# Performance work log

Measured on AMD Instinct MI355X. Metric: run time of the kernel, lower is better.

Reference implementation:

```python
import jax, jax.numpy as jnp
import numpy as np

NEG_SLOPE = 0.2
N, E, NNZ, IN, H, C = 100000, 50000, 800000, 128, 8, 16


def setup_inputs() -> dict:
    key = jax.random.key(0)
    ks = jax.random.split(key, 8)
    X = jax.random.normal(ks[0], (N, IN), jnp.float32)
    W_typed = jax.random.normal(ks[1], (4, IN, H * C), jnp.float32) * (1.0 / np.sqrt(IN))
    att_e = jax.random.normal(ks[2], (4, H, C), jnp.float32) * 0.1
    att_v = jax.random.normal(ks[3], (4, H, C), jnp.float32) * 0.1
    vertex = jax.random.randint(ks[4], (NNZ,), 0, N, jnp.int32)
    edges = jax.random.randint(ks[5], (NNZ,), 0, E, jnp.int32)
    vtype = jax.random.randint(ks[6], (N,), 0, 4, jnp.int32)
    etype = jax.random.randint(ks[7], (E,), 0, 4, jnp.int32)
    return {"X": X, "W_typed": W_typed, "att_e": att_e, "att_v": att_v,
            "vertex": vertex, "edges": edges, "vtype": vtype, "etype": etype}


def _segment_softmax(logits, seg, num):
    # numerically-stable softmax over segments (PyG-style, eps in denominator)
    m = jax.ops.segment_max(logits, seg, num_segments=num)
    ex = jnp.exp(logits - m[seg])
    s = jax.ops.segment_sum(ex, seg, num_segments=num)
    return ex / (s[seg] + 1e-16)


def reference(X, W_typed, att_e, att_v, vertex, edges, vtype, etype):
    # typed linear: project with all 4 type weights, select per node type
    Xall = jnp.einsum('ni,tio->tno', X, W_typed)        # [4, N, H*C]
    X0 = Xall[vtype, jnp.arange(N)]                     # [N, H*C]
    Xn = X0.reshape(N, H, C)
    Xve = Xn[vertex]                                    # [NNZ, H, C] gather vertex->incidence
    # vertex->edge attention, typed by edge type of each incidence
    beta = jnp.sum(Xve * att_e[etype[edges]], axis=-1)  # [NNZ, H]
    beta = jax.nn.leaky_relu(beta, NEG_SLOPE)
    beta = _segment_softmax(beta, edges, E)
    Xe = jax.nn.relu(jax.ops.segment_sum(Xve * beta[..., None], edges, num_segments=E))  # [E, H, C]
    Xe = Xe[edges]                                      # [NNZ, H, C] gather edge->incidence
    # edge->vertex attention, typed by node type of each incidence's vertex
    alpha = jnp.sum(Xe * att_v[vtype[vertex]], axis=-1)  # [NNZ, H]
    alpha = jax.nn.leaky_relu(alpha, NEG_SLOPE)
    alpha = _segment_softmax(alpha, vertex, N)
    Xv = jax.ops.segment_sum(Xe * alpha[..., None], vertex, num_segments=N)  # [N, H, C]
    return Xv.reshape(N, H * C)
```

## Files before the change

kernel.cpp:

```cpp
#include <hip/hip_runtime.h>

typedef __attribute__((ext_vector_type(8))) short bf16x8;
typedef __attribute__((ext_vector_type(4))) float f32x4;

#define NEG_SLOPE 0.2f

__device__ __forceinline__ unsigned short f2bf(float f){
  unsigned u = __float_as_uint(f);
  u = (u + 0x7fffu + ((u >> 16) & 1u)) >> 16;
  return (unsigned short)u;
}
__device__ __forceinline__ float bflo(unsigned u){ return __uint_as_float(u << 16); }
__device__ __forceinline__ float bfhi(unsigned u){ return __uint_as_float(u & 0xffff0000u); }
__device__ __forceinline__ float lrelu(float x){ return x > 0.f ? x : NEG_SLOPE * x; }

__global__ __launch_bounds__(256) void k_histprep(
    const int* __restrict__ edges, const int* __restrict__ vertex, int NNZ,
    int* __restrict__ cnt, int E, int nbHist,
    const int* __restrict__ vtype, int N, int* __restrict__ tcnt, int nbHN,
    const float* __restrict__ W, short* __restrict__ Bfrag){
  __shared__ int lcnt[4];
  int b = (int)blockIdx.x;
  if (b < nbHist){
    int i = b * 256 + threadIdx.x;
    if (i < NNZ){
      atomicAdd(cnt + edges[i], 1);
      atomicAdd(cnt + E + vertex[i], 1);
    }
    return;
  }
  b -= nbHist;
  if (b < nbHN){
    if (threadIdx.x < 4) lcnt[threadIdx.x] = 0;
    __syncthreads();
    int i = b * 256 + threadIdx.x;
    if (i < N) atomicAdd(&lcnt[vtype[i]], 1);
    __syncthreads();
    if (threadIdx.x < 4 && lcnt[threadIdx.x] > 0)
      atomicAdd(tcnt + threadIdx.x, lcnt[threadIdx.x]);
    return;
  }
  b -= nbHN;
  int u = b * 256 + threadIdx.x;
  int j = u & 7, lane = (u >> 3) & 63, ct = (u >> 9) & 31, ks = u >> 14;
  int k = ks * 32 + ((lane >> 4) << 3) + j;
  int col = (ct << 4) + (lane & 15);
  int t = col >> 7, o = col & 127;
  Bfrag[u] = (short)f2bf(W[(t * 128 + k) * 128 + o]);
}

__global__ __launch_bounds__(256) void k_scanA(const int* __restrict__ cnt, int S,
                                               int* __restrict__ bsum){
  __shared__ int sh[256];
  int base = blockIdx.x * 1024 + threadIdx.x * 4;
  int s = 0;
  #pragma unroll
  for (int k = 0; k < 4; ++k){ int idx = base + k; if (idx < S) s += cnt[idx]; }
  sh[threadIdx.x] = s; __syncthreads();
  for (int off = 128; off > 0; off >>= 1){
    if (threadIdx.x < off) sh[threadIdx.x] += sh[threadIdx.x + off];
    __syncthreads();
  }
  if (threadIdx.x == 0) bsum[blockIdx.x] = sh[0];
}

__global__ void k_scanB(int* bsum, int nb, const int* __restrict__ tcnt,
                        int* __restrict__ pbase){
  if (threadIdx.x == 0 && blockIdx.x == 0){
    int run = 0;
    for (int b = 0; b < nb; ++b){ int v = bsum[b]; bsum[b] = run; run += v; }
    int pb = 0;
    for (int t = 0; t < 4; ++t){
      pbase[t] = pb;
      pb += ((tcnt[t] + 63) >> 6) << 6;
    }
    pbase[4] = pb;
  }
}

__global__ __launch_bounds__(256) void k_scanC(const int* __restrict__ cnt, int S,
    const int* __restrict__ bsum, int* __restrict__ offs, int* __restrict__ cursor,
    int nbS, const int* __restrict__ vtype, int N, const int* __restrict__ pbase,
    int* __restrict__ tcur, int* __restrict__ nsorted){
  __shared__ int sh[256];
  __shared__ int gbase[4];
  int t = threadIdx.x;
  int b = (int)blockIdx.x;
  if (b >= nbS){
    int* lcnt = sh;
    if (t < 4) lcnt[t] = 0;
    __syncthreads();
    int i = (b - nbS) * 256 + t;
    int tt = 0, rank = 0;
    bool valid = i < N;
    if (valid){ tt = vtype[i]; rank = atomicAdd(&lcnt[tt], 1); }
    __syncthreads();
    if (t < 4 && lcnt[t] > 0) gbase[t] = atomicAdd(tcur + t, lcnt[t]);
    __syncthreads();
    if (valid) nsorted[pbase[tt] + gbase[tt] + rank] = i;
    return;
  }
  int base = b * 1024 + t * 4;
  int c[4]; int s = 0;
  #pragma unroll
  for (int k = 0; k < 4; ++k){ int idx = base + k; c[k] = (idx < S) ? cnt[idx] : 0; s += c[k]; }
  sh[t] = s; __syncthreads();
  for (int off = 1; off < 256; off <<= 1){
    int v = (t >= off) ? sh[t - off] : 0; __syncthreads();
    sh[t] += v; __syncthreads();
  }
  int run = bsum[b] + sh[t] - s;
  #pragma unroll
  for (int k = 0; k < 4; ++k){
    int idx = base + k;
    if (idx < S){ offs[idx] = run; cursor[idx] = run; run += c[k]; }
  }
}

__global__ __launch_bounds__(256, 3) void k_gemm_place(const float* __restrict__ X,
    const short* __restrict__ Bfrag, const int* __restrict__ nsorted,
    const int* __restrict__ pbase, unsigned short* __restrict__ X0,
    const int* __restrict__ edges, const int* __restrict__ vertex, int NNZ,
    int* __restrict__ cursor, int* __restrict__ rows, int nbPlace){
  __shared__ short shB[8 * 4 * 64 * 8];
  const int tid = threadIdx.x;
  const int q = (int)blockIdx.x / 3, r = (int)blockIdx.x % 3;

  if (r != 0){
    int hb = 2 * q + (r - 1);
    if (hb < nbPlace){
      int i = hb * 256 + tid;
      if (i < NNZ){
        int pos = atomicAdd(cursor + edges[i], 1);
        rows[pos] = vertex[i];
      }
    }
    return;
  }

  const int rowIdx = q * 64;
  const int t = (rowIdx >= pbase[1]) + (rowIdx >= pbase[2]) + (rowIdx >= pbase[3]);

  const bf16x8* Bv = (const bf16x8*)Bfrag;
  bf16x8* shBv = (bf16x8*)shB;
  #pragma unroll
  for (int v = 0; v < 8; ++v){
    int item = v * 256 + tid;
    int slab = item >> 6, ln = item & 63;
    int ks = slab >> 3, ctl = slab & 7;
    shBv[item] = Bv[((ks * 32 + 8 * t + ctl) * 64) + ln];
  }

  const int w = tid >> 6, lane = tid & 63;
  const int m = lane & 15, qq = lane >> 4;
  const int node = nsorted[rowIdx + w * 16 + m];

  bf16x8 afrag[4];
  #pragma unroll
  for (int ks = 0; ks < 4; ++ks){
    bf16x8 f;
    if (node >= 0){
      const float4* src = (const float4*)(X + (size_t)node * 128 + ks * 32 + qq * 8);
      float4 a = src[0], b = src[1];
      f[0]=(short)f2bf(a.x); f[1]=(short)f2bf(a.y); f[2]=(short)f2bf(a.z); f[3]=(short)f2bf(a.w);
      f[4]=(short)f2bf(b.x); f[5]=(short)f2bf(b.y); f[6]=(short)f2bf(b.z); f[7]=(short)f2bf(b.w);
    } else {
      #pragma unroll
      for (int z = 0; z < 8; ++z) f[z] = 0;
    }
    afrag[ks] = f;
  }

  f32x4 acc[8];
  #pragma unroll
  for (int ct = 0; ct < 8; ++ct){
    acc[ct][0]=0.f; acc[ct][1]=0.f; acc[ct][2]=0.f; acc[ct][3]=0.f;
  }

  __syncthreads();
  #pragma unroll
  for (int ctl = 0; ctl < 8; ++ctl){
    #pragma unroll
    for (int ks = 0; ks < 4; ++ks){
      bf16x8 bf = shBv[(ks * 8 + ctl) * 64 + lane];
      acc[ctl] = __builtin_amdgcn_mfma_f32_16x16x32_bf16(afrag[ks], bf, acc[ctl], 0, 0, 0);
    }
  }

  const int col0 = lane & 15;
  #pragma unroll
  for (int rr = 0; rr < 4; ++rr){
    int row = nsorted[rowIdx + w * 16 + qq * 4 + rr];
    if (row < 0) continue;
    #pragma unroll
    for (int ctl = 0; ctl < 8; ++ctl)
      X0[(size_t)row * 128 + ctl * 16 + col0] = f2bf(acc[ctl][rr]);
  }
}

template<int OUT_BF16>
__device__ __forceinline__ void seg_body(const uint4* __restrict__ feat,
    const float* __restrict__ att, const int* __restrict__ rows_sorted,
    const int* __restrict__ offs, const int* __restrict__ cnt,
    const int* __restrict__ stype, void* __restrict__ outbuf,
    int S, int blockId, int tid){
  int wid = tid >> 6, lane = tid & 63;
  int s = blockId * 4 + wid;
  if (s >= S) return;
  int t = stype[s];
  int sub = lane >> 4, lane16 = lane & 15;
  const float4* ap = (const float4*)(att + t * 128 + lane16 * 8);
  float4 A0 = ap[0], A1 = ap[1];
  int start = offs[s], len = cnt[s];
  float denom = 0.f;
  float acc[8];
  #pragma unroll
  for (int e = 0; e < 8; ++e) acc[e] = 0.f;

  for (int base = 0; base < len; base += 64){
    int m = len - base; if (m > 64) m = 64;
    int idx = 0;
    if (lane < m) idx = rows_sorted[start + base + lane];
    int ng = (m + 3) >> 2;
    uint4 uA = make_uint4(0,0,0,0), uB = make_uint4(0,0,0,0);
    {
      int r0 = __shfl(idx, sub);
      if (sub < m) uA = feat[(size_t)r0 * 16 + lane16];
      int r1 = __shfl(idx, 4 + sub);
      if (4 + sub < m) uB = feat[(size_t)r1 * 16 + lane16];
    }
    for (int g = 0; g < ng; g += 2){
      {
        uint4 u = uA;
        int nr = (g + 2) * 4 + sub;
        int rn = __shfl(idx, nr & 63);
        if (nr < m) uA = feat[(size_t)rn * 16 + lane16];
        float x0 = bflo(u.x), x1 = bfhi(u.x), x2 = bflo(u.y), x3 = bfhi(u.y);
        float x4 = bflo(u.z), x5 = bfhi(u.z), x6 = bflo(u.w), x7 = bfhi(u.w);
        float p = x0*A0.x + x1*A0.y + x2*A0.z + x3*A0.w
                + x4*A1.x + x5*A1.y + x6*A1.z + x7*A1.w;
        p += __shfl_xor(p, 1);
        float wgt = __expf(lrelu(p));
        wgt = (g * 4 + sub < m) ? wgt : 0.f;
        denom += wgt;
        acc[0] += wgt*x0; acc[1] += wgt*x1; acc[2] += wgt*x2; acc[3] += wgt*x3;
        acc[4] += wgt*x4; acc[5] += wgt*x5; acc[6] += wgt*x6; acc[7] += wgt*x7;
      }
      if (g + 1 < ng){
        uint4 u = uB;
        int nr = (g + 3) * 4 + sub;
        int rn = __shfl(idx, nr & 63);
        if (nr < m) uB = feat[(size_t)rn * 16 + lane16];
        float x0 = bflo(u.x), x1 = bfhi(u.x), x2 = bflo(u.y), x3 = bfhi(u.y);
        float x4 = bflo(u.z), x5 = bfhi(u.z), x6 = bflo(u.w), x7 = bfhi(u.w);
        float p = x0*A0.x + x1*A0.y + x2*A0.z + x3*A0.w
                + x4*A1.x + x5*A1.y + x6*A1.z + x7*A1.w;
        p += __shfl_xor(p, 1);
        float wgt = __expf(lrelu(p));
        wgt = ((g + 1) * 4 + sub < m) ? wgt : 0.f;
        denom += wgt;
        acc[0] += wgt*x0; acc[1] += wgt*x1; acc[2] += wgt*x2; acc[3] += wgt*x3;
        acc[4] += wgt*x4; acc[5] += wgt*x5; acc[6] += wgt*x6; acc[7] += wgt*x7;
      }
    }
  }
  denom += __shfl_xor(denom, 16);
  denom += __shfl_xor(denom, 32);
  #pragma unroll
  for (int e = 0; e < 8; ++e){
    acc[e] += __shfl_xor(acc[e], 16);
    acc[e] += __shfl_xor(acc[e], 32);
  }
  float inv = 1.f / (denom + 1e-16f);
  float v[8];
  #pragma unroll
  for (int e = 0; e < 8; ++e) v[e] = acc[e] * inv;

  if constexpr (OUT_BF16){
    if (sub == 0){
      uint4 pw;
      pw.x = (unsigned)f2bf(fmaxf(v[0],0.f)) | ((unsigned)f2bf(fmaxf(v[1],0.f)) << 16);
      pw.y = (unsigned)f2bf(fmaxf(v[2],0.f)) | ((unsigned)f2bf(fmaxf(v[3],0.f)) << 16);
      pw.z = (unsigned)f2bf(fmaxf(v[4],0.f)) | ((unsigned)f2bf(fmaxf(v[5],0.f)) << 16);
      pw.w = (unsigned)f2bf(fmaxf(v[6],0.f)) | ((unsigned)f2bf(fmaxf(v[7],0.f)) << 16);
      ((uint4*)outbuf)[(size_t)s * 16 + lane16] = pw;
    }
  } else {
    if (sub == 0){
      float4* op = (float4*)outbuf;
      op[(size_t)s * 32 + lane16 * 2]     = make_float4(v[0], v[1], v[2], v[3]);
      op[(size_t)s * 32 + lane16 * 2 + 1] = make_float4(v[4], v[5], v[6], v[7]);
    }
  }
}

__global__ __launch_bounds__(256) void k_place_seg1(
    const int* __restrict__ edges, const int* __restrict__ vertex, int NNZ,
    int* __restrict__ cursor, int* __restrict__ rows, int E,
    int nbPlace, int nbSeg,
    const uint4* __restrict__ X0, const float* __restrict__ att_e,
    const int* __restrict__ offs, const int* __restrict__ cnt,
    const int* __restrict__ etype, void* __restrict__ Xe){
  const int q = (int)blockIdx.x / 5, r = (int)blockIdx.x % 5;
  if (r == 0){
    if (q < nbPlace){
      int i = q * 256 + threadIdx.x;
      if (i < NNZ){
        int pos = atomicAdd(cursor + E + vertex[i], 1);
        rows[pos] = edges[i];
      }
    }
    return;
  }
  int segBlk = q * 4 + (r - 1);
  if (segBlk >= nbSeg) return;
  seg_body<1>(X0, att_e, rows, offs, cnt, etype, Xe, E, segBlk, threadIdx.x);
}

__global__ __launch_bounds__(256) void k_seg2(const uint4* __restrict__ Xe,
    const float* __restrict__ att_v, const int* __restrict__ rows,
    const int* __restrict__ offs, const int* __restrict__ cnt,
    const int* __restrict__ vtype, float* __restrict__ out, int N){
  seg_body<0>(Xe, att_v, rows, offs, cnt, vtype, out, N,
              (int)blockIdx.x, threadIdx.x);
}

extern "C" void kernel_launch(void* const* d_in, const int* in_sizes, int n_in,
                              void* d_out, int out_size, void* d_ws, size_t ws_size,
                              hipStream_t stream){
  const float* X      = (const float*)d_in[0];
  const float* W      = (const float*)d_in[1];
  const float* att_e  = (const float*)d_in[2];
  const float* att_v  = (const float*)d_in[3];
  const int*   vertex = (const int*)d_in[4];
  const int*   edges  = (const int*)d_in[5];
  const int*   vtype  = (const int*)d_in[6];
  const int*   etype  = (const int*)d_in[7];
  float* out = (float*)d_out;
  const int N   = in_sizes[0] / 128;
  const int NNZ = in_sizes[4];
  const int E   = in_sizes[7];
  const int S   = E + N;

  const int nbI = (NNZ + 255) / 256;
  const int nbHN = (N + 255) / 256;
  const int nbS = (S + 1023) / 1024;
  const int nbSeg1 = (E + 3) / 4;
  const int nbPad = (N + 252 + 63) / 64;
  const int nsortedCap = nbPad * 64;

  char* wp = (char*)d_ws;
  int* cnt    = (int*)wp; wp += (size_t)S * 4;
  int* tcnt   = (int*)wp; wp += 16;
  int* tcur   = (int*)wp; wp += 16;
  int* offs   = (int*)wp; wp += (size_t)S * 4;
  int* cursor = (int*)wp; wp += (size_t)S * 4;
  int* bsum   = (int*)wp; wp += 1024;
  int* pbase  = (int*)wp; wp += 32;
  int* rows   = (int*)wp; wp += (size_t)2 * NNZ * 4;
  int* nsorted= (int*)wp; wp += (size_t)nsortedCap * 4;
  unsigned short* X0 = (unsigned short*)wp; wp += (size_t)N * 128 * 2;
  unsigned short* Xe = (unsigned short*)wp; wp += (size_t)E * 128 * 2;
  short* Bfrag = (short*)wp; wp += (size_t)65536 * 2;

  hipMemsetAsync(cnt, 0, (size_t)(S + 8) * 4, stream);
  hipMemsetAsync(nsorted, 0xFF, (size_t)nsortedCap * 4, stream);

  k_histprep<<<nbI + nbHN + 256, 256, 0, stream>>>(edges, vertex, NNZ, cnt, E,
      nbI, vtype, N, tcnt, nbHN, W, Bfrag);

  k_scanA<<<nbS, 256, 0, stream>>>(cnt, S, bsum);
  k_scanB<<<1, 64, 0, stream>>>(bsum, nbS, tcnt, pbase);
  k_scanC<<<nbS + nbHN, 256, 0, stream>>>(cnt, S, bsum, offs, cursor,
      nbS, vtype, N, pbase, tcur, nsorted);

  k_gemm_place<<<3 * nbPad, 256, 0, stream>>>(X, Bfrag, nsorted, pbase,
      (unsigned short*)X0, edges, vertex, NNZ, cursor, rows, nbI);

  k_place_seg1<<<5 * nbI, 256, 0, stream>>>(edges, vertex, NNZ, cursor,
      rows, E, nbI, nbSeg1, (const uint4*)X0, att_e, offs, cnt, etype, Xe);

  k_seg2<<<(N + 3) / 4, 256, 0, stream>>>((const uint4*)Xe, att_v,
      rows, offs + E, cnt + E, vtype, out, N);
}
```

Baseline: 346.5 us.

## Record histogram ranks during GEMM and place CSR rows without atomics

The edge/vertex histogram now runs alongside the typed-projection GEMM and records each incidence's atomic rank. A separate non-atomic placement kernel then writes rows from offset plus rank, replacing the cursor atomics that previously ran during GEMM and seg1. The node-type sort moves ahead of the GEMM, so the schedule gains kernels (prep, pbase, nodeplace, scan, place) and two NNZ-sized rank buffers. The aim is to drop one round of contended atomics and let the scan overlap less critical work, at the cost of extra launches and memory traffic.

```diff
diff --git a/kernel.cpp b/kernel.cpp
--- a/kernel.cpp
+++ b/kernel.cpp
@@ -14,22 +14,11 @@
 __device__ __forceinline__ float bfhi(unsigned u){ return __uint_as_float(u & 0xffff0000u); }
 __device__ __forceinline__ float lrelu(float x){ return x > 0.f ? x : NEG_SLOPE * x; }
 
-__global__ __launch_bounds__(256) void k_histprep(
-    const int* __restrict__ edges, const int* __restrict__ vertex, int NNZ,
-    int* __restrict__ cnt, int E, int nbHist,
+__global__ __launch_bounds__(256) void k_prep(
     const int* __restrict__ vtype, int N, int* __restrict__ tcnt, int nbHN,
     const float* __restrict__ W, short* __restrict__ Bfrag){
   __shared__ int lcnt[4];
   int b = (int)blockIdx.x;
-  if (b < nbHist){
-    int i = b * 256 + threadIdx.x;
-    if (i < NNZ){
-      atomicAdd(cnt + edges[i], 1);
-      atomicAdd(cnt + E + vertex[i], 1);
-    }
-    return;
-  }
-  b -= nbHist;
   if (b < nbHN){
     if (threadIdx.x < 4) lcnt[threadIdx.x] = 0;
     __syncthreads();
@@ -49,26 +38,8 @@
   Bfrag[u] = (short)f2bf(W[(t * 128 + k) * 128 + o]);
 }
 
-__global__ __launch_bounds__(256) void k_scanA(const int* __restrict__ cnt, int S,
-                                               int* __restrict__ bsum){
-  __shared__ int sh[256];
-  int base = blockIdx.x * 1024 + threadIdx.x * 4;
-  int s = 0;
-  #pragma unroll
-  for (int k = 0; k < 4; ++k){ int idx = base + k; if (idx < S) s += cnt[idx]; }
-  sh[threadIdx.x] = s; __syncthreads();
-  for (int off = 128; off > 0; off >>= 1){
-    if (threadIdx.x < off) sh[threadIdx.x] += sh[threadIdx.x + off];
-    __syncthreads();
-  }
-  if (threadIdx.x == 0) bsum[blockIdx.x] = sh[0];
-}
-
-__global__ void k_scanB(int* bsum, int nb, const int* __restrict__ tcnt,
-                        int* __restrict__ pbase){
+__global__ void k_pbase(const int* __restrict__ tcnt, int* __restrict__ pbase){
   if (threadIdx.x == 0 && blockIdx.x == 0){
-    int run = 0;
-    for (int b = 0; b < nb; ++b){ int v = bsum[b]; bsum[b] = run; run += v; }
     int pb = 0;
     for (int t = 0; t < 4; ++t){
       pbase[t] = pb;
@@ -78,61 +49,41 @@
   }
 }
 
-__global__ __launch_bounds__(256) void k_scanC(const int* __restrict__ cnt, int S,
-    const int* __restrict__ bsum, int* __restrict__ offs, int* __restrict__ cursor,
-    int nbS, const int* __restrict__ vtype, int N, const int* __restrict__ pbase,
+__global__ __launch_bounds__(256) void k_nodeplace(
+    const int* __restrict__ vtype, int N, const int* __restrict__ pbase,
     int* __restrict__ tcur, int* __restrict__ nsorted){
-  __shared__ int sh[256];
+  __shared__ int lcnt[4];
   __shared__ int gbase[4];
   int t = threadIdx.x;
-  int b = (int)blockIdx.x;
-  if (b >= nbS){
-    int* lcnt = sh;
-    if (t < 4) lcnt[t] = 0;
-    __syncthreads();
-    int i = (b - nbS) * 256 + t;
-    int tt = 0, rank = 0;
-    bool valid = i < N;
-    if (valid){ tt = vtype[i]; rank = atomicAdd(&lcnt[tt], 1); }
-    __syncthreads();
-    if (t < 4 && lcnt[t] > 0) gbase[t] = atomicAdd(tcur + t, lcnt[t]);
-    __syncthreads();
-    if (valid) nsorted[pbase[tt] + gbase[tt] + rank] = i;
-    return;
-  }
-  int base = b * 1024 + t * 4;
-  int c[4]; int s = 0;
-  #pragma unroll
-  for (int k = 0; k < 4; ++k){ int idx = base + k; c[k] = (idx < S) ? cnt[idx] : 0; s += c[k]; }
-  sh[t] = s; __syncthreads();
-  for (int off = 1; off < 256; off <<= 1){
-    int v = (t >= off) ? sh[t - off] : 0; __syncthreads();
-    sh[t] += v; __syncthreads();
-  }
-  int run = bsum[b] + sh[t] - s;
-  #pragma unroll
-  for (int k = 0; k < 4; ++k){
-    int idx = base + k;
-    if (idx < S){ offs[idx] = run; cursor[idx] = run; run += c[k]; }
-  }
-}
-
-__global__ __launch_bounds__(256, 3) void k_gemm_place(const float* __restrict__ X,
+  if (t < 4) lcnt[t] = 0;
+  __syncthreads();
+  int i = (int)blockIdx.x * 256 + t;
+  int tt = 0, rank = 0;
+  bool valid = i < N;
+  if (valid){ tt = vtype[i]; rank = atomicAdd(&lcnt[tt], 1); }
+  __syncthreads();
+  if (t < 4 && lcnt[t] > 0) gbase[t] = atomicAdd(tcur + t, lcnt[t]);
+  __syncthreads();
+  if (valid) nsorted[pbase[tt] + gbase[tt] + rank] = i;
+}
+
+__global__ __launch_bounds__(256, 3) void k_gemm_hist(const float* __restrict__ X,
     const short* __restrict__ Bfrag, const int* __restrict__ nsorted,
     const int* __restrict__ pbase, unsigned short* __restrict__ X0,
     const int* __restrict__ edges, const int* __restrict__ vertex, int NNZ,
-    int* __restrict__ cursor, int* __restrict__ rows, int nbPlace){
+    int* __restrict__ cnt, int E,
+    int* __restrict__ rank_e, int* __restrict__ rank_v, int nbHist){
   __shared__ short shB[8 * 4 * 64 * 8];
   const int tid = threadIdx.x;
   const int q = (int)blockIdx.x / 3, r = (int)blockIdx.x % 3;
 
   if (r != 0){
     int hb = 2 * q + (r - 1);
-    if (hb < nbPlace){
+    if (hb < nbHist){
       int i = hb * 256 + tid;
       if (i < NNZ){
-        int pos = atomicAdd(cursor + edges[i], 1);
-        rows[pos] = vertex[i];
+        rank_e[i] = atomicAdd(cnt + edges[i], 1);
+        rank_v[i] = atomicAdd(cnt + E + vertex[i], 1);
       }
     }
     return;
@@ -196,6 +147,61 @@
     for (int ctl = 0; ctl < 8; ++ctl)
       X0[(size_t)row * 128 + ctl * 16 + col0] = f2bf(acc[ctl][rr]);
   }
+}
+
+__global__ __launch_bounds__(256) void k_scanA(const int* __restrict__ cnt, int S,
+                                               int* __restrict__ bsum){
+  __shared__ int sh[256];
+  int base = blockIdx.x * 1024 + threadIdx.x * 4;
+  int s = 0;
+  #pragma unroll
+  for (int k = 0; k < 4; ++k){ int idx = base + k; if (idx < S) s += cnt[idx]; }
+  sh[threadIdx.x] = s; __syncthreads();
+  for (int off = 128; off > 0; off >>= 1){
+    if (threadIdx.x < off) sh[threadIdx.x] += sh[threadIdx.x + off];
+    __syncthreads();
+  }
+  if (threadIdx.x == 0) bsum[blockIdx.x] = sh[0];
+}
+
+__global__ void k_scanB2(int* bsum, int nb){
+  if (threadIdx.x == 0 && blockIdx.x == 0){
+    int run = 0;
+    for (int b = 0; b < nb; ++b){ int v = bsum[b]; bsum[b] = run; run += v; }
+  }
+}
+
+__global__ __launch_bounds__(256) void k_scanC2(const int* __restrict__ cnt, int S,
+    const int* __restrict__ bsum, int* __restrict__ offs){
+  __shared__ int sh[256];
+  int t = threadIdx.x;
+  int b = (int)blockIdx.x;
+  int base = b * 1024 + t * 4;
+  int c[4]; int s = 0;
+  #pragma unroll
+  for (int k = 0; k < 4; ++k){ int idx = base + k; c[k] = (idx < S) ? cnt[idx] : 0; s += c[k]; }
+  sh[t] = s; __syncthreads();
+  for (int off = 1; off < 256; off <<= 1){
+    int v = (t >= off) ? sh[t - off] : 0; __syncthreads();
+    sh[t] += v; __syncthreads();
+  }
+  int run = bsum[b] + sh[t] - s;
+  #pragma unroll
+  for (int k = 0; k < 4; ++k){
+    int idx = base + k;
+    if (idx < S){ offs[idx] = run; run += c[k]; }
+  }
+}
+
+__global__ __launch_bounds__(256) void k_place(
+    const int* __restrict__ edges, const int* __restrict__ vertex, int NNZ,
+    const int* __restrict__ offs, const int* __restrict__ rank_e,
+    const int* __restrict__ rank_v, int* __restrict__ rows, int E){
+  int q = (int)blockIdx.x >> 1, r = (int)blockIdx.x & 1;
+  int i = q * 256 + (int)threadIdx.x;
+  if (i >= NNZ) return;
+  if (r == 0) rows[offs[edges[i]]      + rank_e[i]] = vertex[i];
+  else        rows[offs[E + vertex[i]] + rank_v[i]] = edges[i];
 }
 
 template<int OUT_BF16>
@@ -294,27 +300,12 @@
   }
 }
 
-__global__ __launch_bounds__(256) void k_place_seg1(
-    const int* __restrict__ edges, const int* __restrict__ vertex, int NNZ,
-    int* __restrict__ cursor, int* __restrict__ rows, int E,
-    int nbPlace, int nbSeg,
-    const uint4* __restrict__ X0, const float* __restrict__ att_e,
+__global__ __launch_bounds__(256) void k_seg1(const uint4* __restrict__ X0,
+    const float* __restrict__ att_e, const int* __restrict__ rows,
     const int* __restrict__ offs, const int* __restrict__ cnt,
-    const int* __restrict__ etype, void* __restrict__ Xe){
-  const int q = (int)blockIdx.x / 5, r = (int)blockIdx.x % 5;
-  if (r == 0){
-    if (q < nbPlace){
-      int i = q * 256 + threadIdx.x;
-      if (i < NNZ){
-        int pos = atomicAdd(cursor + E + vertex[i], 1);
-        rows[pos] = edges[i];
-      }
-    }
-    return;
-  }
-  int segBlk = q * 4 + (r - 1);
-  if (segBlk >= nbSeg) return;
-  seg_body<1>(X0, att_e, rows, offs, cnt, etype, Xe, E, segBlk, threadIdx.x);
+    const int* __restrict__ etype, void* __restrict__ Xe, int E){
+  seg_body<1>(X0, att_e, rows, offs, cnt, etype, Xe, E,
+              (int)blockIdx.x, threadIdx.x);
 }
 
 __global__ __launch_bounds__(256) void k_seg2(const uint4* __restrict__ Xe,
@@ -354,11 +345,12 @@
   int* tcnt   = (int*)wp; wp += 16;
   int* tcur   = (int*)wp; wp += 16;
   int* offs   = (int*)wp; wp += (size_t)S * 4;
-  int* cursor = (int*)wp; wp += (size_t)S * 4;
   int* bsum   = (int*)wp; wp += 1024;
   int* pbase  = (int*)wp; wp += 32;
   int* rows   = (int*)wp; wp += (size_t)2 * NNZ * 4;
   int* nsorted= (int*)wp; wp += (size_t)nsortedCap * 4;
+  int* rank_e = (int*)wp; wp += (size_t)NNZ * 4;
+  int* rank_v = (int*)wp; wp += (size_t)NNZ * 4;
   unsigned short* X0 = (unsigned short*)wp; wp += (size_t)N * 128 * 2;
   unsigned short* Xe = (unsigned short*)wp; wp += (size_t)E * 128 * 2;
   short* Bfrag = (short*)wp; wp += (size_t)65536 * 2;
@@ -366,19 +358,22 @@
   hipMemsetAsync(cnt, 0, (size_t)(S + 8) * 4, stream);
   hipMemsetAsync(nsorted, 0xFF, (size_t)nsortedCap * 4, stream);
 
-  k_histprep<<<nbI + nbHN + 256, 256, 0, stream>>>(edges, vertex, NNZ, cnt, E,
-      nbI, vtype, N, tcnt, nbHN, W, Bfrag);
+  k_prep<<<nbHN + 256, 256, 0, stream>>>(vtype, N, tcnt, nbHN, W, Bfrag);
+  k_pbase<<<1, 64, 0, stream>>>(tcnt, pbase);
+  k_nodeplace<<<nbHN, 256, 0, stream>>>(vtype, N, pbase, tcur, nsorted);
+
+  k_gemm_hist<<<3 * nbPad, 256, 0, stream>>>(X, Bfrag, nsorted, pbase,
+      (unsigned short*)X0, edges, vertex, NNZ, cnt, E, rank_e, rank_v, nbI);
 
   k_scanA<<<nbS, 256, 0, stream>>>(cnt, S, bsum);
-  k_scanB<<<1, 64, 0, stream>>>(bsum, nbS, tcnt, pbase);
-  k_scanC<<<nbS + nbHN, 256, 0, stream>>>(cnt, S, bsum, offs, cursor,
-      nbS, vtype, N, pbase, tcur, nsorted);
-
-  k_gemm_place<<<3 * nbPad, 256, 0, stream>>>(X, Bfrag, nsorted, pbase,
-      (unsigned short*)X0, edges, vertex, NNZ, cursor, rows, nbI);
-
-  k_place_seg1<<<5 * nbI, 256, 0, stream>>>(edges, vertex, NNZ, cursor,
-      rows, E, nbI, nbSeg1, (const uint4*)X0, att_e, offs, cnt, etype, Xe);
+  k_scanB2<<<1, 64, 0, stream>>>(bsum, nbS);
+  k_scanC2<<<nbS, 256, 0, stream>>>(cnt, S, bsum, offs);
+
+  k_place<<<2 * nbI, 256, 0, stream>>>(edges, vertex, NNZ, offs,
+      rank_e, rank_v, rows, E);
+
+  k_seg1<<<nbSeg1, 256, 0, stream>>>((const uint4*)X0, att_e, rows,
+      offs, cnt, etype, Xe, E);
 
   k_seg2<<<(N + 3) / 4, 256, 0, stream>>>((const uint4*)Xe, att_v,
       rows, offs + E, cnt + E, vtype, out, N);
```

Result: faster. 316.6 us (-8.6%).
